# Performance work log

Measured on AMD Instinct MI355X. Metric: run time of the kernel, lower is better.

The kernel has to match this reference:

```python
import jax, jax.numpy as jnp
from jax import lax
import numpy as np

B, L, D, KSIZE = 8, 2048, 256, 8


def setup_inputs() -> dict:
    key = jax.random.key(0)
    kx, kw, kwin, kb, ktau = jax.random.split(key, 5)
    scale = 1.0 / np.sqrt(D).astype(np.float32)
    x = jax.random.normal(kx, (B, L, D), dtype=jnp.float32)
    weight = jax.random.normal(kw, (D, D), dtype=jnp.float32) * scale
    input_weight = jax.random.normal(kwin, (D, D), dtype=jnp.float32) * scale
    bias = jax.random.normal(kb, (1, D), dtype=jnp.float32)
    # tau = |randn| in the original; offset by 1 to keep 1/tau numerically sane
    tau = jnp.abs(jax.random.normal(ktau, (1, D), dtype=jnp.float32)) + 1.0
    return {"x": x, "weight": weight, "input_weight": input_weight,
            "bias": bias, "tau": tau, "ksize": KSIZE}


def reference(x, weight, input_weight, bias, tau, ksize):
    b, l, d = x.shape
    # get_K: left-pad with (ksize-1) zeros, gather overlapping windows
    xp = jnp.pad(x, ((0, 0), (ksize - 1, 0), (0, 0)))
    idx = jnp.arange(l)[:, None] + jnp.arange(ksize)[None, :]  # (l, ksize)
    windows = xp[:, idx, :]                                    # (b, l, ksize, d)
    xw = windows.reshape(b * l, ksize, d)                      # flatten per-window batch

    inv_tau = 1.0 / tau                                        # (1, d)
    h0 = jnp.zeros((b * l, d), dtype=x.dtype)

    def step(h, xt):
        # SimpleCTRNN update: h += (1/tau) * (-h + relu(h W + x W_in + b))
        h_new = h + inv_tau * (-h + jax.nn.relu(h @ weight + xt @ input_weight + bias))
        return h_new, None

    xs = jnp.swapaxes(xw, 0, 1)                                # (ksize, b*l, d)
    h_last, _ = lax.scan(step, h0, xs)
    # forward() keeps only the last window timestep
    return h_last.reshape(b, l, d)
```

## Files before the change

### kernel.cpp

```cpp
#include <hip/hip_runtime.h>

typedef __bf16 bf16_t;
typedef __bf16 bf16x8 __attribute__((ext_vector_type(8)));
typedef float  f32x4  __attribute__((ext_vector_type(4)));

#define Bdim 8
#define Ldim 2048
#define Ddim 256
#define MROWS 64
#define USTRIDE 84

__global__ void swz_kernel(const float* __restrict__ w,
                           const float* __restrict__ win,
                           bf16_t* __restrict__ wsw,
                           bf16_t* __restrict__ winsw) {
    int tid  = blockIdx.x * blockDim.x + threadIdx.x;
    int mat  = tid >> 16;
    int e    = tid & 65535;
    int j    = e & 7;
    int lane = (e >> 3) & 63;
    int nt   = (e >> 9) & 15;
    int kt   = e >> 13;
    int c = lane & 15, q = lane >> 4;
    int k = kt * 32 + q * 8 + j;
    int n = nt * 16 + c;
    const float* src = mat ? win : w;
    bf16_t v = (bf16_t)src[k * Ddim + n];
    if (mat) winsw[e] = v; else wsw[e] = v;
}

__global__ __launch_bounds__(256, 1)
void rnn_kernel(const float* __restrict__ x,
                const float* __restrict__ bias,
                const float* __restrict__ tau,
                const bf16x8* __restrict__ wsw,
                const bf16x8* __restrict__ winsw,
                float* __restrict__ out)
{
    __shared__ float  Ut[Ddim * USTRIDE];
    __shared__ bf16_t hbuf[4 * 8 * 64 * 8];

    const int tid = threadIdx.x;
    const int w   = tid >> 6;
    const int ln  = tid & 63;
    const int c   = ln & 15;
    const int q   = ln >> 4;
    const int blk = blockIdx.x;
    const int bb  = blk >> 5;
    const int l0  = (blk & 31) * MROWS;

    int   ncol[4];
    float itau[4];
#pragma unroll
    for (int nl = 0; nl < 4; ++nl) {
        ncol[nl] = (4 * w + nl) * 16 + c;
        itau[nl] = 1.0f / tau[ncol[nl]];
    }

    bf16x8 bfr[8][4];
#pragma unroll
    for (int kt = 0; kt < 8; ++kt)
#pragma unroll
        for (int nl = 0; nl < 4; ++nl)
            bfr[kt][nl] = winsw[(kt * 16 + 4 * w + nl) * 64 + ln];

    f32x4 au[5][4];
#pragma unroll
    for (int nl = 0; nl < 4; ++nl) {
        float bv = bias[ncol[nl]];
#pragma unroll
        for (int mt = 0; mt < 5; ++mt) {
            f32x4 t = {bv, bv, bv, bv};
            au[mt][nl] = t;
        }
    }

    const float* xb = x + bb * (Ldim * Ddim);
#pragma unroll
    for (int kt = 0; kt < 8; ++kt) {
        bf16x8 aF[5];
#pragma unroll
        for (int mt = 0; mt < 5; ++mt) {
            int lrow = l0 - 7 + mt * 16 + c;
            f32x4 a0 = {0.f, 0.f, 0.f, 0.f};
            f32x4 a1 = {0.f, 0.f, 0.f, 0.f};
            if (lrow >= 0 && lrow < Ldim) {
                const f32x4* p = (const f32x4*)(xb + lrow * Ddim + kt * 32 + q * 8);
                a0 = p[0];
                a1 = p[1];
            }
            bf16x8 av;
#pragma unroll
            for (int jj = 0; jj < 4; ++jj) {
                av[jj]     = (bf16_t)a0[jj];
                av[jj + 4] = (bf16_t)a1[jj];
            }
            aF[mt] = av;
        }
#pragma unroll
        for (int nl = 0; nl < 4; ++nl)
#pragma unroll
            for (int mt = 0; mt < 5; ++mt)
                au[mt][nl] = __builtin_amdgcn_mfma_f32_16x16x32_bf16(
                    aF[mt], bfr[kt][nl], au[mt][nl], 0, 0, 0);
    }

#pragma unroll
    for (int mt = 0; mt < 5; ++mt)
#pragma unroll
        for (int nl = 0; nl < 4; ++nl)
            *(f32x4*)&Ut[ncol[nl] * USTRIDE + mt * 16 + 4 * q] = au[mt][nl];

    __syncthreads();

#pragma unroll
    for (int kt = 0; kt < 8; ++kt)
#pragma unroll
        for (int nl = 0; nl < 4; ++nl)
            bfr[kt][nl] = wsw[(kt * 16 + 4 * w + nl) * 64 + ln];

    f32x4 h[4][4];
#pragma unroll
    for (int mt = 0; mt < 4; ++mt)
#pragma unroll
        for (int nl = 0; nl < 4; ++nl)
#pragma unroll
            for (int r = 0; r < 4; ++r) {
                float u = Ut[ncol[nl] * USTRIDE + mt * 16 + 4 * q + r];
                h[mt][nl][r] = itau[nl] * fmaxf(u, 0.0f);
            }

#pragma unroll 1
    for (int t = 1; t < 8; ++t) {
#pragma unroll
        for (int mt = 0; mt < 4; ++mt)
#pragma unroll
            for (int nl = 0; nl < 4; ++nl) {
                int kk  = ncol[nl];
                int ktg = kk >> 5;
                int qp  = (kk >> 3) & 3;
                int jj  = kk & 7;
#pragma unroll
                for (int r = 0; r < 4; ++r) {
                    int m = 4 * q + r;
                    hbuf[(mt * 8 + ktg) * 512 + ((qp << 4) + m) * 8 + jj] =
                        (bf16_t)h[mt][nl][r];
                }
            }
        f32x4 acc[4][4];
#pragma unroll
        for (int mt = 0; mt < 4; ++mt)
#pragma unroll
            for (int nl = 0; nl < 4; ++nl)
#pragma unroll
                for (int r = 0; r < 4; ++r)
                    acc[mt][nl][r] =
                        Ut[ncol[nl] * USTRIDE + mt * 16 + 4 * q + r + t];
        __syncthreads();
#pragma unroll
        for (int kt = 0; kt < 8; ++kt) {
            bf16x8 aF[4];
#pragma unroll
            for (int mt = 0; mt < 4; ++mt)
                aF[mt] = *(const bf16x8*)&hbuf[(mt * 8 + kt) * 512 + ln * 8];
#pragma unroll
            for (int nl = 0; nl < 4; ++nl)
#pragma unroll
                for (int mt = 0; mt < 4; ++mt)
                    acc[mt][nl] = __builtin_amdgcn_mfma_f32_16x16x32_bf16(
                        aF[mt], bfr[kt][nl], acc[mt][nl], 0, 0, 0);
        }
        __syncthreads();
#pragma unroll
        for (int mt = 0; mt < 4; ++mt)
#pragma unroll
            for (int nl = 0; nl < 4; ++nl)
#pragma unroll
                for (int r = 0; r < 4; ++r) {
                    float hh = h[mt][nl][r];
                    float s  = fmaxf(acc[mt][nl][r], 0.0f);
                    h[mt][nl][r] = hh + itau[nl] * (s - hh);
                }
    }

    float* ob = out + (bb * Ldim + l0) * Ddim;
#pragma unroll
    for (int mt = 0; mt < 4; ++mt)
#pragma unroll
        for (int nl = 0; nl < 4; ++nl)
#pragma unroll
            for (int r = 0; r < 4; ++r)
                ob[(mt * 16 + 4 * q + r) * Ddim + ncol[nl]] = h[mt][nl][r];
}

extern "C" void kernel_launch(void* const* d_in, const int* in_sizes, int n_in,
                              void* d_out, int out_size, void* d_ws, size_t ws_size,
                              hipStream_t stream) {
    const float* x            = (const float*)d_in[0];
    const float* weight       = (const float*)d_in[1];
    const float* input_weight = (const float*)d_in[2];
    const float* bias         = (const float*)d_in[3];
    const float* tau          = (const float*)d_in[4];
    (void)in_sizes; (void)n_in; (void)out_size; (void)ws_size;

    bf16_t* wsw   = (bf16_t*)d_ws;
    bf16_t* winsw = wsw + 65536;

    swz_kernel<<<512, 256, 0, stream>>>(weight, input_weight, wsw, winsw);
    rnn_kernel<<<256, 256, 0, stream>>>(x, bias, tau,
                                        (const bf16x8*)wsw, (const bf16x8*)winsw,
                                        (float*)d_out);
}
```

Baseline: 110.9 us.

## Keep input projection in registers with shuffles, pipeline x loads, vectorize weight swizzle

Removes the large shared-memory Ut buffer holding the input projection. The projection now stays in registers, and each step shifts it by one timestep using lane shuffles, with the shifted value seeding the first MFMA accumulator. The input-projection GEMM double-buffers its x and weight loads across k-tiles, the hbuf writes and reads use precomputed and permuted byte offsets, and the swizzle kernel writes vectorized bf16x8 from 16 blocks instead of scalar elements from 512. The goal is to cut LDS traffic and footprint and to overlap global loads with MFMA, at the cost of more register pressure and shuffle logic.

```diff
diff --git a/kernel.cpp b/kernel.cpp
--- a/kernel.cpp
+++ b/kernel.cpp
@@ -4,29 +4,28 @@
 typedef __bf16 bf16x8 __attribute__((ext_vector_type(8)));
 typedef float  f32x4  __attribute__((ext_vector_type(4)));
 
-#define Bdim 8
 #define Ldim 2048
 #define Ddim 256
 #define MROWS 64
-#define USTRIDE 84
 
 __global__ void swz_kernel(const float* __restrict__ w,
                            const float* __restrict__ win,
                            bf16_t* __restrict__ wsw,
                            bf16_t* __restrict__ winsw) {
-    int tid  = blockIdx.x * blockDim.x + threadIdx.x;
-    int mat  = tid >> 16;
-    int e    = tid & 65535;
-    int j    = e & 7;
-    int lane = (e >> 3) & 63;
-    int nt   = (e >> 9) & 15;
-    int kt   = e >> 13;
-    int c = lane & 15, q = lane >> 4;
-    int k = kt * 32 + q * 8 + j;
-    int n = nt * 16 + c;
+    int mat = blockIdx.x >> 3, kt = blockIdx.x & 7;
     const float* src = mat ? win : w;
-    bf16_t v = (bf16_t)src[k * Ddim + n];
-    if (mat) winsw[e] = v; else wsw[e] = v;
+    bf16_t*      dst = mat ? winsw : wsw;
+    int ln = threadIdx.x & 63, g = threadIdx.x >> 6;
+    int c = ln & 15, q = ln >> 4;
+#pragma unroll
+    for (int i = 0; i < 4; ++i) {
+        int nt = g + 4 * i;
+        bf16x8 v;
+#pragma unroll
+        for (int j = 0; j < 8; ++j)
+            v[j] = (bf16_t)src[(kt * 32 + q * 8 + j) * Ddim + nt * 16 + c];
+        *(bf16x8*)&dst[((kt * 16 + nt) * 64 + ln) * 8] = v;
+    }
 }
 
 __global__ __launch_bounds__(256, 1)
@@ -37,8 +36,8 @@
                 const bf16x8* __restrict__ winsw,
                 float* __restrict__ out)
 {
-    __shared__ float  Ut[Ddim * USTRIDE];
-    __shared__ bf16_t hbuf[4 * 8 * 64 * 8];
+    __shared__ bf16_t hbuf[4 * 8 * 512];
+    char* hb = (char*)hbuf;
 
     const int tid = threadIdx.x;
     const int w   = tid >> 6;
@@ -57,13 +56,6 @@
         itau[nl] = 1.0f / tau[ncol[nl]];
     }
 
-    bf16x8 bfr[8][4];
-#pragma unroll
-    for (int kt = 0; kt < 8; ++kt)
-#pragma unroll
-        for (int nl = 0; nl < 4; ++nl)
-            bfr[kt][nl] = winsw[(kt * 16 + 4 * w + nl) * 64 + ln];
-
     f32x4 au[5][4];
 #pragma unroll
     for (int nl = 0; nl < 4; ++nl) {
@@ -75,100 +67,117 @@
         }
     }
 
-    const float* xb = x + bb * (Ldim * Ddim);
-#pragma unroll
-    for (int kt = 0; kt < 8; ++kt) {
+    const float* xb = x + (long)bb * (Ldim * Ddim);
+    const f32x4 zf = {0.f, 0.f, 0.f, 0.f};
+
+    auto loadX = [&](f32x4 (&buf)[5][2], int kt) {
+#pragma unroll
+        for (int mt = 0; mt < 5; ++mt) {
+            int  lrow = l0 - 7 + mt * 16 + c;
+            bool ok   = (lrow >= 0) && (lrow < Ldim);
+            const f32x4* p = (const f32x4*)(xb + (long)lrow * Ddim + kt * 32 + q * 8);
+            buf[mt][0] = ok ? p[0] : zf;
+            buf[mt][1] = ok ? p[1] : zf;
+        }
+    };
+    auto loadW = [&](bf16x8 (&wb)[4], int kt) {
+#pragma unroll
+        for (int nl = 0; nl < 4; ++nl)
+            wb[nl] = winsw[(kt * 16 + 4 * w + nl) * 64 + ln];
+    };
+    auto step1 = [&](const f32x4 (&buf)[5][2], const bf16x8 (&wb)[4]) {
         bf16x8 aF[5];
 #pragma unroll
-        for (int mt = 0; mt < 5; ++mt) {
-            int lrow = l0 - 7 + mt * 16 + c;
-            f32x4 a0 = {0.f, 0.f, 0.f, 0.f};
-            f32x4 a1 = {0.f, 0.f, 0.f, 0.f};
-            if (lrow >= 0 && lrow < Ldim) {
-                const f32x4* p = (const f32x4*)(xb + lrow * Ddim + kt * 32 + q * 8);
-                a0 = p[0];
-                a1 = p[1];
+        for (int mt = 0; mt < 5; ++mt)
+#pragma unroll
+            for (int jj = 0; jj < 4; ++jj) {
+                aF[mt][jj]     = (bf16_t)buf[mt][0][jj];
+                aF[mt][jj + 4] = (bf16_t)buf[mt][1][jj];
             }
-            bf16x8 av;
-#pragma unroll
-            for (int jj = 0; jj < 4; ++jj) {
-                av[jj]     = (bf16_t)a0[jj];
-                av[jj + 4] = (bf16_t)a1[jj];
-            }
-            aF[mt] = av;
-        }
 #pragma unroll
         for (int nl = 0; nl < 4; ++nl)
 #pragma unroll
             for (int mt = 0; mt < 5; ++mt)
                 au[mt][nl] = __builtin_amdgcn_mfma_f32_16x16x32_bf16(
-                    aF[mt], bfr[kt][nl], au[mt][nl], 0, 0, 0);
-    }
-
-#pragma unroll
-    for (int mt = 0; mt < 5; ++mt)
-#pragma unroll
-        for (int nl = 0; nl < 4; ++nl)
-            *(f32x4*)&Ut[ncol[nl] * USTRIDE + mt * 16 + 4 * q] = au[mt][nl];
-
-    __syncthreads();
-
+                    aF[mt], wb[nl], au[mt][nl], 0, 0, 0);
+    };
+
+    {
+        f32x4  x0[5][2], x1[5][2];
+        bf16x8 w0[4], w1[4];
+        loadX(x0, 0); loadW(w0, 0);
+#pragma unroll 1
+        for (int kk = 0; kk < 4; ++kk) {
+            loadX(x1, 2 * kk + 1); loadW(w1, 2 * kk + 1);
+            step1(x0, w0);
+            if (kk < 3) { loadX(x0, 2 * kk + 2); loadW(w0, 2 * kk + 2); }
+            step1(x1, w1);
+        }
+    }
+
+    bf16x8 bfr[8][4];
 #pragma unroll
     for (int kt = 0; kt < 8; ++kt)
 #pragma unroll
         for (int nl = 0; nl < 4; ++nl)
             bfr[kt][nl] = wsw[(kt * 16 + 4 * w + nl) * 64 + ln];
 
+    int offn[4];
+#pragma unroll
+    for (int nl = 0; nl < 4; ++nl) {
+        int kk = ncol[nl];
+        offn[nl] = (kk >> 5) * 1024 + ((kk >> 3) & 3) * 64 + q * 16 + (kk & 7) * 2;
+    }
+    const int permln = (((ln & 3) << 4) | ((ln >> 4) << 2) | ((ln >> 2) & 3)) * 16;
+    const int sl     = (ln + 16) & 63;
+
     f32x4 h[4][4];
 #pragma unroll
     for (int mt = 0; mt < 4; ++mt)
 #pragma unroll
         for (int nl = 0; nl < 4; ++nl)
 #pragma unroll
-            for (int r = 0; r < 4; ++r) {
-                float u = Ut[ncol[nl] * USTRIDE + mt * 16 + 4 * q + r];
-                h[mt][nl][r] = itau[nl] * fmaxf(u, 0.0f);
-            }
+            for (int r = 0; r < 4; ++r)
+                h[mt][nl][r] = itau[nl] * fmaxf(au[mt][nl][r], 0.0f);
 
 #pragma unroll 1
     for (int t = 1; t < 8; ++t) {
 #pragma unroll
+        for (int nl = 0; nl < 4; ++nl) {
+            float a[5];
+#pragma unroll
+            for (int mt = 0; mt < 5; ++mt) a[mt] = __shfl(au[mt][nl][0], sl);
+#pragma unroll
+            for (int mt = 0; mt < 5; ++mt) {
+                float n3 = (q < 3) ? a[mt] : (mt < 4 ? a[mt + 1] : a[mt]);
+                f32x4 o = au[mt][nl];
+                f32x4 s = {o[1], o[2], o[3], n3};
+                au[mt][nl] = s;
+            }
+        }
+#pragma unroll
         for (int mt = 0; mt < 4; ++mt)
 #pragma unroll
-            for (int nl = 0; nl < 4; ++nl) {
-                int kk  = ncol[nl];
-                int ktg = kk >> 5;
-                int qp  = (kk >> 3) & 3;
-                int jj  = kk & 7;
-#pragma unroll
-                for (int r = 0; r < 4; ++r) {
-                    int m = 4 * q + r;
-                    hbuf[(mt * 8 + ktg) * 512 + ((qp << 4) + m) * 8 + jj] =
+            for (int nl = 0; nl < 4; ++nl)
+#pragma unroll
+                for (int r = 0; r < 4; ++r)
+                    *(bf16_t*)(hb + mt * 8192 + r * 256 + offn[nl]) =
                         (bf16_t)h[mt][nl][r];
-                }
-            }
+        __syncthreads();
         f32x4 acc[4][4];
-#pragma unroll
-        for (int mt = 0; mt < 4; ++mt)
-#pragma unroll
-            for (int nl = 0; nl < 4; ++nl)
-#pragma unroll
-                for (int r = 0; r < 4; ++r)
-                    acc[mt][nl][r] =
-                        Ut[ncol[nl] * USTRIDE + mt * 16 + 4 * q + r + t];
-        __syncthreads();
 #pragma unroll
         for (int kt = 0; kt < 8; ++kt) {
             bf16x8 aF[4];
 #pragma unroll
             for (int mt = 0; mt < 4; ++mt)
-                aF[mt] = *(const bf16x8*)&hbuf[(mt * 8 + kt) * 512 + ln * 8];
+                aF[mt] = *(const bf16x8*)(hb + (mt * 8 + kt) * 1024 + permln);
 #pragma unroll
             for (int nl = 0; nl < 4; ++nl)
 #pragma unroll
                 for (int mt = 0; mt < 4; ++mt)
                     acc[mt][nl] = __builtin_amdgcn_mfma_f32_16x16x32_bf16(
-                        aF[mt], bfr[kt][nl], acc[mt][nl], 0, 0, 0);
+                        aF[mt], bfr[kt][nl],
+                        (kt == 0) ? au[mt][nl] : acc[mt][nl], 0, 0, 0);
         }
         __syncthreads();
 #pragma unroll
@@ -183,7 +192,7 @@
                 }
     }
 
-    float* ob = out + (bb * Ldim + l0) * Ddim;
+    float* ob = out + ((long)bb * Ldim + l0) * Ddim;
 #pragma unroll
     for (int mt = 0; mt < 4; ++mt)
 #pragma unroll
@@ -206,7 +215,7 @@
     bf16_t* wsw   = (bf16_t*)d_ws;
     bf16_t* winsw = wsw + 65536;
 
-    swz_kernel<<<512, 256, 0, stream>>>(weight, input_weight, wsw, winsw);
+    swz_kernel<<<16, 256, 0, stream>>>(weight, input_weight, wsw, winsw);
     rnn_kernel<<<256, 256, 0, stream>>>(x, bias, tau,
                                         (const bf16x8*)wsw, (const bf16x8*)winsw,
                                         (float*)d_out);
```

New measurement: 108.0 us. -2.7%, faster.
